# Kernel optimization log

Measured on AMD Instinct MI355X. Metric: run time of the kernel, lower is better.

The kernel has to match this reference:

```python
import jax, jax.numpy as jnp
import numpy as np

M = 12          # grid size (m)
BIG = 1e10      # Dijkstra initial_cost default
EPS = 1e-5      # BatchNorm eps

def _conv(x, w, stride, pad):
    return jax.lax.conv_general_dilated(x, w, (stride, stride), [(pad, pad), (pad, pad)],
                                        dimension_numbers=('NCHW', 'OIHW', 'NCHW'))

def _bn(x, g, b, m, v):
    # eval-mode batchnorm with running stats
    return (x - m[:, None, None]) * (g[:, None, None] * jax.lax.rsqrt(v[:, None, None] + EPS)) + b[:, None, None]

def _maxpool(x):
    return jax.lax.reduce_window(x, -jnp.inf, jax.lax.max, (1, 1, 3, 3), (1, 1, 2, 2),
                                 [(0, 0), (0, 0), (1, 1), (1, 1)])

def _basic_block(x, w1, g1, b1, m1, v1, w2, g2, b2, m2, v2):
    y = jax.nn.relu(_bn(_conv(x, w1, 1, 1), g1, b1, m1, v1))
    y = _bn(_conv(y, w2, 1, 1), g2, b2, m2, v2)
    return jax.nn.relu(x + y)

def _relax(dist, costs):
    # Bellman-Ford relaxation on 4-neighbor grid with vertex costs
    pad_r = jnp.full((1, M), BIG, dist.dtype)
    pad_c = jnp.full((M, 1), BIG, dist.dtype)
    up = jnp.concatenate([pad_r, dist[:-1]], 0)
    down = jnp.concatenate([dist[1:], pad_r], 0)
    left = jnp.concatenate([pad_c, dist[:, :-1]], 1)
    right = jnp.concatenate([dist[:, 1:], pad_c], 1)
    nbr = jnp.minimum(jnp.minimum(up, down), jnp.minimum(left, right))
    return jnp.minimum(dist, nbr + costs)

def _shortest_path(costs):
    # single-sample shortest path (0,0)->(M-1,M-1); returns binary path indicator [M,M]
    dist = jnp.full((M, M), BIG, costs.dtype).at[0, 0].set(costs[0, 0])
    dist = jax.lax.fori_loop(0, M * M, lambda t, d: _relax(d, costs), dist)
    offs = jnp.array([[-1, 0], [1, 0], [0, -1], [0, 1]], jnp.int32)

    def body(t, carry):
        mask, i, j = carry
        mask = mask.at[i, j].set(jnp.asarray(1.0, mask.dtype))
        ni = i + offs[:, 0]
        nj = j + offs[:, 1]
        valid = (ni >= 0) & (ni < M) & (nj >= 0) & (nj < M)
        vals = jnp.where(valid, dist[jnp.clip(ni, 0, M - 1), jnp.clip(nj, 0, M - 1)], BIG)
        k = jnp.argmin(vals)
        at_start = (i == 0) & (j == 0)
        i2 = jnp.where(at_start, i, ni[k])
        j2 = jnp.where(at_start, j, nj[k])
        return mask, i2, j2

    init = (jnp.zeros((M, M), costs.dtype), jnp.int32(M - 1), jnp.int32(M - 1))
    mask, _, _ = jax.lax.fori_loop(0, M * M, body, init)
    return mask

def setup_inputs() -> dict:
    key = jax.random.key(0)
    ks = jax.random.split(key, 4)
    x = jax.random.normal(ks[0], (128, 3, 96, 96), jnp.float32)
    conv1_w = jax.random.normal(ks[1], (64, 3, 7, 7), jnp.float32) * 0.05
    blk_w = jax.random.normal(ks[2], (4, 64, 64, 3, 3), jnp.float32) * 0.05
    fc_w = jax.random.normal(ks[3], (M * M, 64 * 24 * 24), jnp.float32) * 0.01
    return {
        'x': x,
        'conv1_w': conv1_w,
        'bn1_g': jnp.ones(64), 'bn1_b': jnp.zeros(64), 'bn1_m': jnp.zeros(64), 'bn1_v': jnp.ones(64),
        'blk_w': blk_w,
        'blk_g': jnp.ones((4, 64)), 'blk_b': jnp.zeros((4, 64)),
        'blk_m': jnp.zeros((4, 64)), 'blk_v': jnp.ones((4, 64)),
        'fc_w': fc_w, 'fc_b': jnp.zeros(M * M),
    }

def reference(x, conv1_w, bn1_g, bn1_b, bn1_m, bn1_v, blk_w, blk_g, blk_b, blk_m, blk_v, fc_w, fc_b):
    h = jax.nn.relu(_bn(_conv(x, conv1_w, 2, 3), bn1_g, bn1_b, bn1_m, bn1_v))
    h = _maxpool(h)  # [B,64,24,24]
    for blk in range(2):  # resnet18 layer1: two BasicBlocks
        a, b2 = 2 * blk, 2 * blk + 1
        h = _basic_block(h,
                         blk_w[a], blk_g[a], blk_b[a], blk_m[a], blk_v[a],
                         blk_w[b2], blk_g[b2], blk_b[b2], blk_m[b2], blk_v[b2])
    cost_vec = h.reshape(h.shape[0], -1) @ fc_w.T + fc_b  # [B, m*m]
    costs = cost_vec.reshape(-1, M, M)
    path = jax.vmap(_shortest_path)(costs)  # [B, m, m] binary
    return path
```

## Files before the change

kernel.cpp:

```cpp
#include <hip/hip_runtime.h>
#include <math.h>

#define BIGF 1e10f
#define EPSF 1e-5f

typedef _Float16 f16;
typedef f16 f16x8 __attribute__((ext_vector_type(8)));
typedef float f32x4 __attribute__((ext_vector_type(4)));

static __device__ __forceinline__ f16x8 mk8(uint a, uint b, uint c, uint d) {
    union { uint u[4]; f16x8 v; } t;
    t.u[0] = a; t.u[1] = b; t.u[2] = c; t.u[3] = d;
    return t.v;
}

__global__ __launch_bounds__(256) void prepack(
    const float* __restrict__ c1w,
    const float* __restrict__ bn1g, const float* __restrict__ bn1b,
    const float* __restrict__ bn1m, const float* __restrict__ bn1v,
    const float* __restrict__ blkw,
    const float* __restrict__ blkg, const float* __restrict__ blkb,
    const float* __restrict__ blkm, const float* __restrict__ blkv,
    f16* __restrict__ wB, f16* __restrict__ wB1,
    float* __restrict__ b3, float* __restrict__ b1)
{
    int idx = blockIdx.x * 256 + threadIdx.x;
    if (idx < 147456) {
        int pos = idx;
        int j    = pos & 7;
        int lane = (pos >> 3) & 63;
        int rest = pos >> 9;
        int kf   = rest & 1;
        int r2   = rest >> 1;
        int ntl  = r2 & 3;
        int r3   = r2 >> 2;
        int tap  = r3 % 9;
        int layer= r3 / 9;
        int ic = kf * 32 + (lane >> 4) * 8 + j;
        int oc = ntl * 16 + (lane & 15);
        float s = blkg[layer * 64 + oc] * rsqrtf(blkv[layer * 64 + oc] + EPSF);
        float wv = blkw[(((size_t)layer * 64 + oc) * 64 + ic) * 9 + tap] * s;
        f16 h = (f16)wv;
        f16 lo = (f16)(wv - (float)h);
        int low9 = pos & 511;
        wB[(size_t)rest * 1024 + low9]       = h;
        wB[(size_t)rest * 1024 + 512 + low9] = lo;
    }
    int q = idx - 147456;
    if (q >= 0 && q < 28672) {
        int j = q & 7, lane = (q >> 3) & 63, rest = q >> 9;
        int hl = rest & 1, nt = (rest >> 1) & 3, kh = rest >> 3;
        int oc = nt * 16 + (lane & 15), lgq = lane >> 4;
        float v = 0.f;
        if (lgq < 3 && j < 7) {
            float s = bn1g[oc] * rsqrtf(bn1v[oc] + EPSF);
            v = c1w[((oc * 3 + lgq) * 7 + kh) * 7 + j] * s;
        }
        f16 h = (f16)v;
        wB1[q] = hl ? (f16)(v - (float)h) : h;
    }
    int k = idx - 147456 - 28672;
    if (k >= 0 && k < 256) {
        float s = blkg[k] * rsqrtf(blkv[k] + EPSF);
        b3[k] = blkb[k] - blkm[k] * s;
    }
    int l = idx - 147456 - 28672 - 256;
    if (l >= 0 && l < 64) {
        float s = bn1g[l] * rsqrtf(bn1v[l] + EPSF);
        b1[l] = bn1b[l] - bn1m[l] * s;
    }
}

__global__ __launch_bounds__(256) void conv1_mfma(
    const float* __restrict__ x, const f16* __restrict__ wB1,
    const float* __restrict__ bias,
    f16* __restrict__ outh, f16* __restrict__ outl)
{
    __shared__ char lds[18720];
    const int g = blockIdx.x, b = blockIdx.y;
    const int tid = threadIdx.x;
    const int w = tid >> 6, l = tid & 63;
    const int l15 = l & 15, lg = l >> 4;

    for (int i = tid; i < 4680; i += 256) ((uint*)lds)[i] = 0u;
    __syncthreads();
    const int ir0 = 8 * g - 5;
    const float* xb = x + (size_t)b * 27648;
    for (int u = tid; u < 2205; u += 256) {
        int cu = 1 + (u % 49);
        int rr = (u / 49) % 15;
        int ic = u / 735;
        int ir = ir0 + rr;
        uint pk_h = 0u, pk_l = 0u;
        if ((unsigned)ir < 96u) {
            int c0i = 2 * cu - 3, c1i = 2 * cu - 2;
            const float* rowp = xb + ic * 9216 + ir * 96;
            float v0 = (c0i >= 0) ? rowp[c0i] : 0.f;
            float v1 = (c1i <= 95) ? rowp[c1i] : 0.f;
            f16 h0 = (f16)v0; f16 lo0 = (f16)(v0 - (float)h0);
            f16 h1 = (f16)v1; f16 lo1 = (f16)(v1 - (float)h1);
            union { f16 f[2]; uint u32; } ph, pl;
            ph.f[0] = h0;  ph.f[1] = h1;  pk_h = ph.u32;
            pl.f[0] = lo0; pl.f[1] = lo1; pk_l = pl.u32;
        }
        int off = ic * 3120 + rr * 208 + 4 * cu;
        *(uint*)(lds + off) = pk_h;
        *(uint*)(lds + 9360 + off) = pk_l;
    }
    __syncthreads();

    f32x4 acc[4][4];
#pragma unroll
    for (int k = 0; k < 4; ++k)
#pragma unroll
        for (int nt = 0; nt < 4; ++nt) acc[k][nt] = (f32x4){0.f, 0.f, 0.f, 0.f};

    const int icB = (lg >= 3 ? 0 : lg) * 3120;
    const char* hbase = lds + icB;
    const char* lbase = lds + 9360 + icB;
    const f16* wq = wB1 + (size_t)l * 8;

    int rowoff[4], aoff[4];
#pragma unroll
    for (int k = 0; k < 4; ++k) {
        int t = w + 4 * k;
        int tt = (t < 15) ? t : 0;
        rowoff[k] = tt / 3;
        aoff[k] = 4 * ((tt % 3) * 16 + l15);
    }

#pragma unroll 1
    for (int kh = 0; kh < 7; ++kh) {
        const f16* wk = wq + kh * 4096;
        f16x8 bq[4];
#pragma unroll
        for (int nt = 0; nt < 4; ++nt)
            bq[nt] = *(const f16x8*)(const void*)(wk + nt * 1024);
#pragma unroll
        for (int k = 0; k < 4; ++k) {
            if (w + 4 * k < 15) {
                int ro = (2 * rowoff[k] + kh) * 208 + aoff[k];
                const uint* ph = (const uint*)(hbase + ro);
                const uint* pl = (const uint*)(lbase + ro);
                f16x8 ah = mk8(ph[0], ph[1], ph[2], ph[3]);
                f16x8 al = mk8(pl[0], pl[1], pl[2], pl[3]);
#pragma unroll
                for (int nt = 0; nt < 4; ++nt) {
                    acc[k][nt] = __builtin_amdgcn_mfma_f32_16x16x32_f16(ah, bq[nt], acc[k][nt], 0, 0, 0);
                    acc[k][nt] = __builtin_amdgcn_mfma_f32_16x16x32_f16(al, bq[nt], acc[k][nt], 0, 0, 0);
                }
            }
        }
#pragma unroll
        for (int nt = 0; nt < 4; ++nt)
            bq[nt] = *(const f16x8*)(const void*)(wk + nt * 1024 + 512);
#pragma unroll
        for (int k = 0; k < 4; ++k) {
            if (w + 4 * k < 15) {
                int ro = (2 * rowoff[k] + kh) * 208 + aoff[k];
                const uint* ph = (const uint*)(hbase + ro);
                f16x8 ah = mk8(ph[0], ph[1], ph[2], ph[3]);
#pragma unroll
                for (int nt = 0; nt < 4; ++nt)
                    acc[k][nt] = __builtin_amdgcn_mfma_f32_16x16x32_f16(ah, bq[nt], acc[k][nt], 0, 0, 0);
            }
        }
    }

    __syncthreads();
    float* pbuf = (float*)(void*)lds;
#pragma unroll
    for (int og = 0; og < 4; ++og) {
        float bi = bias[og * 16 + l15];
#pragma unroll
        for (int k = 0; k < 4; ++k) {
            int t = w + 4 * k;
            if (t < 15) {
                int lr = t / 3;
                int c0 = (t % 3) * 16;
#pragma unroll
                for (int r = 0; r < 4; ++r) {
                    int col = c0 + lg * 4 + r;
                    pbuf[(lr * 48 + col) * 17 + l15] = fmaxf(acc[k][og][r] + bi, 0.f);
                }
            }
        }
        __syncthreads();
#pragma unroll
        for (int it = 0; it < 3; ++it) {
            int idx = tid + it * 256;
            int oc = idx & 15, p2 = idx >> 4;
            int pc2 = p2 % 24, pr2 = p2 / 24;
            float m = -INFINITY;
#pragma unroll
            for (int kr = 0; kr < 3; ++kr) {
                int lr = 2 * pr2 + kr;
                if (g == 0 && lr == 0) continue;
#pragma unroll
                for (int kc = 0; kc < 3; ++kc) {
                    int cc = 2 * pc2 - 1 + kc;
                    if ((unsigned)cc < 48u)
                        m = fmaxf(m, pbuf[(lr * 48 + cc) * 17 + oc]);
                }
            }
            f16 h = (f16)m;
            f16 lo = (f16)(m - (float)h);
            size_t off = (size_t)b * 36864 +
                         (size_t)((2 * g + pr2) * 24 + pc2) * 64 + og * 16 + oc;
            outh[off] = h;
            outl[off] = lo;
        }
        __syncthreads();
    }
}

template<int MODE, int OUTT>
__global__ __launch_bounds__(256) void conv3_mfma(
    const f16* __restrict__ inh, const f16* __restrict__ inl,
    const f16* __restrict__ wB,
    const float* __restrict__ bias,
    const f16* __restrict__ resh, const f16* __restrict__ resl,
    f16* __restrict__ outh, f16* __restrict__ outl)
{
    __shared__ f16 lh[6 * 26 * 64];
    __shared__ f16 ll[6 * 26 * 64];
    const int r0 = blockIdx.x * 4;
    const int b  = blockIdx.y;
    const int tid = threadIdx.x;
    const int w = tid >> 6, l = tid & 63;
    const int l15 = l & 15, lg = l >> 4;

    if (tid < 192) {
        int arr = tid >= 96; int c2 = tid - arr * 96;
        int slot = c2 & 7; int pb = c2 >> 3;
        int lr = pb >> 1; int pc = (pb & 1) ? 25 : 0;
        int pix = lr * 26 + pc;
        int off = (pix * 128 + slot * 16) ^ ((pix & 7) << 4);
        *(uint4*)((arr ? (char*)ll : (char*)lh) + off) = make_uint4(0, 0, 0, 0);
    }
#pragma unroll
    for (int i = 0; i < 9; ++i) {
        int ch = tid + i * 256;
        int arr = ch >= 1152; int c2 = ch - arr * 1152;
        int slot = c2 & 7; int pix24 = c2 >> 3;
        int lr = pix24 / 24, pc = pix24 % 24;
        int ir = r0 - 1 + lr;
        uint4 v = make_uint4(0, 0, 0, 0);
        if ((unsigned)ir < 24u) {
            const f16* src = (arr ? inl : inh) +
                (((size_t)b * 576 + ir * 24 + pc) << 6) + slot * 8;
            v = *(const uint4*)(const void*)src;
        }
        int pix = lr * 26 + pc + 1;
        int off = (pix * 128 + slot * 16) ^ ((pix & 7) << 4);
        *(uint4*)((arr ? (char*)ll : (char*)lh) + off) = v;
    }

    int pr_[2], pc_[2];
#pragma unroll
    for (int mtl = 0; mtl < 2; ++mtl) {
        int t = w + 4 * mtl;
        int tt = (t < 6) ? t : 0;
        int lp = tt * 16 + l15;
        pr_[mtl] = lp / 24; pc_[mtl] = lp % 24;
    }

    f32x4 acc[2][4];
#pragma unroll
    for (int m = 0; m < 2; ++m)
#pragma unroll
        for (int n = 0; n < 4; ++n) acc[m][n] = (f32x4){0.f, 0.f, 0.f, 0.f};

    __syncthreads();

#pragma unroll 1
    for (int tap = 0; tap < 9; ++tap) {
        int dr = tap / 3, dc = tap % 3;
#pragma unroll
        for (int kf = 0; kf < 2; ++kf) {
            const f16* wb = wB + (size_t)tap * 8192 + (size_t)kf * 1024 + (size_t)l * 8;
            f16x8 bh[4], bl[4];
#pragma unroll
            for (int nt = 0; nt < 4; ++nt) {
                bh[nt] = *(const f16x8*)(const void*)(wb + nt * 2048);
                bl[nt] = *(const f16x8*)(const void*)(wb + nt * 2048 + 512);
            }
#pragma unroll
            for (int mtl = 0; mtl < 2; ++mtl) {
                if (mtl == 1 && w >= 2) continue;
                int pix = (pr_[mtl] + dr) * 26 + (pc_[mtl] + dc);
                int off = (pix * 128 + kf * 64 + lg * 16) ^ ((pix & 7) << 4);
                f16x8 ah = *(const f16x8*)((const char*)lh + off);
                f16x8 al = *(const f16x8*)((const char*)ll + off);
#pragma unroll
                for (int nt = 0; nt < 4; ++nt) {
                    acc[mtl][nt] = __builtin_amdgcn_mfma_f32_16x16x32_f16(ah, bh[nt], acc[mtl][nt], 0, 0, 0);
                    acc[mtl][nt] = __builtin_amdgcn_mfma_f32_16x16x32_f16(ah, bl[nt], acc[mtl][nt], 0, 0, 0);
                    acc[mtl][nt] = __builtin_amdgcn_mfma_f32_16x16x32_f16(al, bh[nt], acc[mtl][nt], 0, 0, 0);
                }
            }
        }
    }

    float bi[4];
#pragma unroll
    for (int nt = 0; nt < 4; ++nt) bi[nt] = bias[nt * 16 + l15];

#pragma unroll
    for (int mtl = 0; mtl < 2; ++mtl) {
        if (mtl == 1 && w >= 2) continue;
        int t = w + 4 * mtl;
#pragma unroll
        for (int nt = 0; nt < 4; ++nt) {
#pragma unroll
            for (int r = 0; r < 4; ++r) {
                int lp = t * 16 + lg * 4 + r;
                int p = r0 * 24 + lp;
                int oc = nt * 16 + l15;
                float v = acc[mtl][nt][r] + bi[nt];
                if (MODE) {
                    size_t ridx = (size_t)b * 36864 + (size_t)p * 64 + oc;
                    v += (float)resh[ridx] + (float)resl[ridx];
                }
                v = fmaxf(v, 0.f);
                f16 h = (f16)v;
                f16 lo = (f16)(v - (float)h);
                size_t oidx = OUTT ? ((size_t)b * 36864 + (size_t)oc * 576 + p)
                                   : ((size_t)b * 36864 + (size_t)p * 64 + oc);
                outh[oidx] = h;
                outl[oidx] = lo;
            }
        }
    }
}

#define FC_KSPLIT 32

__global__ __launch_bounds__(256) void fc_mfma(
    const f16* __restrict__ Ath, const f16* __restrict__ Atl,
    const float* __restrict__ Bw, float* __restrict__ part)
{
    __shared__ f16 As[2][128 * 40];
    __shared__ f16 Bs[2][16 * 40];
    const int nt = blockIdx.x;
    const int ks = blockIdx.y;
    const int tid = threadIdx.x;
    const int w = tid >> 6, l = tid & 63;
    const int l15 = l & 15, lg = l >> 4;
    const int k0b = ks * 1152;

    f32x4 acc[2];
    acc[0] = (f32x4){0.f, 0.f, 0.f, 0.f};
    acc[1] = (f32x4){0.f, 0.f, 0.f, 0.f};

    const int bn = tid >> 4, bkl = (tid & 15) * 2;
#pragma unroll 1
    for (int st = 0; st < 36; ++st) {
        int k0 = k0b + st * 32;
        __syncthreads();
#pragma unroll
        for (int i = 0; i < 4; ++i) {
            int ch = tid + i * 256;
            int arr = ch >= 512; int c2 = ch - arr * 512;
            int m = c2 >> 2, slot = c2 & 3;
            const f16* src = (arr ? Atl : Ath) + (size_t)m * 36864 + k0 + slot * 8;
            *(uint4*)(void*)&As[arr][m * 40 + slot * 8] = *(const uint4*)(const void*)src;
        }
        {
            float2 f2 = *(const float2*)&Bw[(size_t)(nt * 16 + bn) * 36864 + k0 + bkl];
            f16 h0 = (f16)f2.x, h1 = (f16)f2.y;
            Bs[0][bn * 40 + bkl] = h0;     Bs[0][bn * 40 + bkl + 1] = h1;
            Bs[1][bn * 40 + bkl] = (f16)(f2.x - (float)h0);
            Bs[1][bn * 40 + bkl + 1] = (f16)(f2.y - (float)h1);
        }
        __syncthreads();
        f16x8 bh = *(const f16x8*)(const void*)&Bs[0][l15 * 40 + lg * 8];
        f16x8 bl = *(const f16x8*)(const void*)&Bs[1][l15 * 40 + lg * 8];
#pragma unroll
        for (int mtl = 0; mtl < 2; ++mtl) {
            int m = w * 32 + mtl * 16 + l15;
            f16x8 ah = *(const f16x8*)(const void*)&As[0][m * 40 + lg * 8];
            f16x8 al = *(const f16x8*)(const void*)&As[1][m * 40 + lg * 8];
            acc[mtl] = __builtin_amdgcn_mfma_f32_16x16x32_f16(ah, bh, acc[mtl], 0, 0, 0);
            acc[mtl] = __builtin_amdgcn_mfma_f32_16x16x32_f16(ah, bl, acc[mtl], 0, 0, 0);
            acc[mtl] = __builtin_amdgcn_mfma_f32_16x16x32_f16(al, bh, acc[mtl], 0, 0, 0);
        }
    }
#pragma unroll
    for (int mtl = 0; mtl < 2; ++mtl)
#pragma unroll
        for (int r = 0; r < 4; ++r) {
            int m = w * 32 + mtl * 16 + lg * 4 + r;
            int n = nt * 16 + l15;
            part[((size_t)ks * 128 + m) * 144 + n] = acc[mtl][r];
        }
}

__global__ __launch_bounds__(256) void fc_reduce(
    const float* __restrict__ part, const float* __restrict__ bias,
    float* __restrict__ costs)
{
    int idx = blockIdx.x * 256 + threadIdx.x;
    if (idx >= 128 * 144) return;
    float sum = bias[idx % 144];
    for (int s = 0; s < FC_KSPLIT; ++s) sum += part[(size_t)s * (128 * 144) + idx];
    costs[idx] = sum;
}

__global__ __launch_bounds__(192) void shortest_path(
    const float* __restrict__ costs, float* __restrict__ out)
{
    __shared__ float dA[144], dB[144], cs[144], mask[144];
    const int b = blockIdx.x, tid = threadIdx.x;
    if (tid < 144) {
        float c = costs[b * 144 + tid];
        cs[tid] = c;
        dA[tid] = (tid == 0) ? c : BIGF;
        mask[tid] = 0.f;
    }
    __syncthreads();
    float* cur = dA; float* nxt = dB;
    for (int it = 0; it < 144; ++it) {
        if (tid < 144) {
            int i = tid / 12, j = tid % 12;
            float up = (i > 0)  ? cur[tid - 12] : BIGF;
            float dn = (i < 11) ? cur[tid + 12] : BIGF;
            float lf = (j > 0)  ? cur[tid - 1]  : BIGF;
            float rt = (j < 11) ? cur[tid + 1]  : BIGF;
            float nb = fminf(fminf(up, dn), fminf(lf, rt));
            nxt[tid] = fminf(cur[tid], nb + cs[tid]);
        }
        __syncthreads();
        float* tp = cur; cur = nxt; nxt = tp;
    }
    if (tid == 0) {
        int i = 11, j = 11;
        const int di[4] = {-1, 1, 0, 0};
        const int dj[4] = {0, 0, -1, 1};
        for (int it = 0; it < 144; ++it) {
            mask[i * 12 + j] = 1.f;
            float vals[4];
#pragma unroll
            for (int k = 0; k < 4; ++k) {
                int ni = i + di[k], nj = j + dj[k];
                bool valid = (ni >= 0) && (ni < 12) && (nj >= 0) && (nj < 12);
                vals[k] = valid ? cur[ni * 12 + nj] : BIGF;
            }
            float best = vals[0]; int kb = 0;
#pragma unroll
            for (int k = 1; k < 4; ++k)
                if (vals[k] < best) { best = vals[k]; kb = k; }
            if (!(i == 0 && j == 0)) { i += di[kb]; j += dj[kb]; }
        }
    }
    __syncthreads();
    if (tid < 144) out[b * 144 + tid] = mask[tid];
}

extern "C" void kernel_launch(void* const* d_in, const int* in_sizes, int n_in,
                              void* d_out, int out_size, void* d_ws, size_t ws_size,
                              hipStream_t stream) {
    const float* x    = (const float*)d_in[0];
    const float* c1w  = (const float*)d_in[1];
    const float* bn1g = (const float*)d_in[2];
    const float* bn1b = (const float*)d_in[3];
    const float* bn1m = (const float*)d_in[4];
    const float* bn1v = (const float*)d_in[5];
    const float* blkw = (const float*)d_in[6];
    const float* blkg = (const float*)d_in[7];
    const float* blkb = (const float*)d_in[8];
    const float* blkm = (const float*)d_in[9];
    const float* blkv = (const float*)d_in[10];
    const float* fcw  = (const float*)d_in[11];
    const float* fcb  = (const float*)d_in[12];
    float* out = (float*)d_out;
    char* ws = (char*)d_ws;

    const size_t APL = 9437184;
    f16* a0h = (f16*)(ws);
    f16* a0l = (f16*)(ws + APL);
    f16* a1h = (f16*)(ws + 2 * APL);
    f16* a1l = (f16*)(ws + 3 * APL);
    f16* a2h = (f16*)(ws + 4 * APL);
    f16* a2l = (f16*)(ws + 5 * APL);
    float* costs = (float*)(ws + 6 * APL);
    float* part  = (float*)(ws + 6 * APL + 73728);
    f16*   wB    = (f16*)  (ws + 6 * APL + 73728 + 2359296);
    float* b3    = (float*)(ws + 6 * APL + 73728 + 2359296 + 589824);
    float* b1    = (float*)(ws + 6 * APL + 73728 + 2359296 + 589824 + 1024);
    f16*   wB1   = (f16*)  (ws + 6 * APL + 73728 + 2359296 + 589824 + 1280);

    prepack<<<dim3(690), dim3(256), 0, stream>>>(
        c1w, bn1g, bn1b, bn1m, bn1v, blkw, blkg, blkb, blkm, blkv,
        wB, wB1, b3, b1);

    conv1_mfma<<<dim3(12, 128), dim3(256), 0, stream>>>(x, wB1, b1, a0h, a0l);

    conv3_mfma<0, 0><<<dim3(6, 128), dim3(256), 0, stream>>>(
        a0h, a0l, wB + 0 * 73728, b3 + 0,   nullptr, nullptr, a1h, a1l);
    conv3_mfma<1, 0><<<dim3(6, 128), dim3(256), 0, stream>>>(
        a1h, a1l, wB + 1 * 73728, b3 + 64,  a0h, a0l, a2h, a2l);
    conv3_mfma<0, 0><<<dim3(6, 128), dim3(256), 0, stream>>>(
        a2h, a2l, wB + 2 * 73728, b3 + 128, nullptr, nullptr, a1h, a1l);
    conv3_mfma<1, 1><<<dim3(6, 128), dim3(256), 0, stream>>>(
        a1h, a1l, wB + 3 * 73728, b3 + 192, a2h, a2l, a0h, a0l);

    fc_mfma<<<dim3(9, FC_KSPLIT), dim3(256), 0, stream>>>(a0h, a0l, fcw, part);
    fc_reduce<<<dim3(72), dim3(256), 0, stream>>>(part, fcb, costs);
    shortest_path<<<dim3(128), dim3(192), 0, stream>>>(costs, out);
}
```

Measured before the change: 238.2 us.

## Fuse two Bellman-Ford relaxation steps per sync with padded shared grid

The shortest-path kernel now stores distances and costs in a 16x16 shared grid padded with BIG values, so boundary checks go away. Each thread evaluates two relaxation steps at once from a 13-point stencil, which halves the loop to 72 iterations and halves the number of barriers. The backtrack loop exits early once it reaches the origin. In exchange, each step does more shared-memory reads and min operations. Results should be the same because two Jacobi steps are computed exactly.

Measured after the change: 222.5 us. -6.6%, faster.

```diff
diff --git a/kernel.cpp b/kernel.cpp
--- a/kernel.cpp
+++ b/kernel.cpp
@@ -410,47 +410,74 @@
 __global__ __launch_bounds__(192) void shortest_path(
     const float* __restrict__ costs, float* __restrict__ out)
 {
-    __shared__ float dA[144], dB[144], cs[144], mask[144];
+    __shared__ float dP[2][256];
+    __shared__ float cP[256];
+    __shared__ float mask[144];
     const int b = blockIdx.x, tid = threadIdx.x;
+
+    if (tid < 128) {
+        dP[0][tid] = BIGF; dP[0][tid + 128] = BIGF;
+        dP[1][tid] = BIGF; dP[1][tid + 128] = BIGF;
+        cP[tid] = BIGF;    cP[tid + 128] = BIGF;
+    }
+    if (tid < 144) mask[tid] = 0.f;
+    __syncthreads();
+
+    const int i = tid / 12, j = tid % 12;
+    const int p = (i + 2) * 16 + (j + 2);
     if (tid < 144) {
         float c = costs[b * 144 + tid];
-        cs[tid] = c;
-        dA[tid] = (tid == 0) ? c : BIGF;
-        mask[tid] = 0.f;
-    }
-    __syncthreads();
-    float* cur = dA; float* nxt = dB;
-    for (int it = 0; it < 144; ++it) {
+        cP[p] = c;
+        if (tid == 0) dP[0][p] = c;
+    }
+    __syncthreads();
+
+    float cS = 0.f, cU = 0.f, cD = 0.f, cL = 0.f, cR = 0.f;
+    if (tid < 144) {
+        cS = cP[p];
+        cU = cP[p - 16]; cD = cP[p + 16];
+        cL = cP[p - 1];  cR = cP[p + 1];
+    }
+
+    int cur = 0;
+#pragma unroll 1
+    for (int it = 0; it < 72; ++it) {
         if (tid < 144) {
-            int i = tid / 12, j = tid % 12;
-            float up = (i > 0)  ? cur[tid - 12] : BIGF;
-            float dn = (i < 11) ? cur[tid + 12] : BIGF;
-            float lf = (j > 0)  ? cur[tid - 1]  : BIGF;
-            float rt = (j < 11) ? cur[tid + 1]  : BIGF;
-            float nb = fminf(fminf(up, dn), fminf(lf, rt));
-            nxt[tid] = fminf(cur[tid], nb + cs[tid]);
+            const float* cb = dP[cur];
+            float dS = cb[p];
+            float dU = cb[p - 16], dD = cb[p + 16], dL = cb[p - 1],  dR = cb[p + 1];
+            float dUU = cb[p - 32], dDD = cb[p + 32], dLL = cb[p - 2], dRR = cb[p + 2];
+            float dUL = cb[p - 17], dUR = cb[p - 15], dDL = cb[p + 15], dDR = cb[p + 17];
+            float ndU = fminf(dU, fminf(fminf(dUU, dS), fminf(dUL, dUR)) + cU);
+            float ndD = fminf(dD, fminf(fminf(dS, dDD), fminf(dDL, dDR)) + cD);
+            float ndL = fminf(dL, fminf(fminf(dUL, dDL), fminf(dLL, dS)) + cL);
+            float ndR = fminf(dR, fminf(fminf(dUR, dDR), fminf(dS, dRR)) + cR);
+            float ndS = fminf(dS, fminf(fminf(dU, dD), fminf(dL, dR)) + cS);
+            float d2 = fminf(ndS, fminf(fminf(ndU, ndD), fminf(ndL, ndR)) + cS);
+            dP[cur ^ 1][p] = d2;
         }
         __syncthreads();
-        float* tp = cur; cur = nxt; nxt = tp;
-    }
+        cur ^= 1;
+    }
+
     if (tid == 0) {
-        int i = 11, j = 11;
-        const int di[4] = {-1, 1, 0, 0};
-        const int dj[4] = {0, 0, -1, 1};
+        const float* fb = dP[cur];
+        int pi = 11, pj = 11;
+#pragma unroll 1
         for (int it = 0; it < 144; ++it) {
-            mask[i * 12 + j] = 1.f;
-            float vals[4];
-#pragma unroll
-            for (int k = 0; k < 4; ++k) {
-                int ni = i + di[k], nj = j + dj[k];
-                bool valid = (ni >= 0) && (ni < 12) && (nj >= 0) && (nj < 12);
-                vals[k] = valid ? cur[ni * 12 + nj] : BIGF;
-            }
-            float best = vals[0]; int kb = 0;
-#pragma unroll
-            for (int k = 1; k < 4; ++k)
-                if (vals[k] < best) { best = vals[k]; kb = k; }
-            if (!(i == 0 && j == 0)) { i += di[kb]; j += dj[kb]; }
+            mask[pi * 12 + pj] = 1.f;
+            if (pi == 0 && pj == 0) break;
+            int pp = (pi + 2) * 16 + (pj + 2);
+            float vu = fb[pp - 16];
+            float vd = fb[pp + 16];
+            float vl = fb[pp - 1];
+            float vr = fb[pp + 1];
+            float best = vu; int kb = 0;
+            if (vd < best) { best = vd; kb = 1; }
+            if (vl < best) { best = vl; kb = 2; }
+            if (vr < best) { best = vr; kb = 3; }
+            pi += (kb == 0) ? -1 : (kb == 1) ? 1 : 0;
+            pj += (kb == 2) ? -1 : (kb == 3) ? 1 : 0;
         }
     }
     __syncthreads();
```
